# Performance work log

Measured on AMD Instinct MI355X. Metric: run time of the kernel, lower is better.

Reference implementation:

```python
import jax, jax.numpy as jnp
import numpy as np
import math


def hs_pe(x, fr, fi):
    # x: [N, c, h, w], c = cp*3; fr/fi: [max_len, cp] real/imag of freqs_cis.
    N, c, h, w = x.shape
    cp = c // 3
    xs = x.reshape(N, cp, 3, h, w)
    a, b, c3 = xs[:, :, 0], xs[:, :, 1], xs[:, :, 2]
    # rotate (a, b) as complex along h axis
    frh = fr[:h].T[None, :, :, None]  # [1, cp, h, 1]
    fih = fi[:h].T[None, :, :, None]
    a2 = a * frh - b * fih
    b2 = a * fih + b * frh
    # rotate (b2, c3) as complex along w axis
    frw = fr[:w].T[None, :, None, :]  # [1, cp, 1, w]
    fiw = fi[:w].T[None, :, None, :]
    b3 = b2 * frw - c3 * fiw
    c32 = b2 * fiw + c3 * frw
    return jnp.stack([a2, b3, c32], axis=2).reshape(N, c, h, w)


def partition(x, ws, dr):
    # OverlapDilatedWindowPartion
    B, C, H, W = x.shape
    Wsz = ws + dr
    st = Wsz // 2
    nh = math.ceil(H / Wsz)
    nw = math.ceil(W / Wsz)
    x = jnp.pad(x, ((0, 0), (0, 0), (0, nh * Wsz - H), (0, nw * Wsz - W)), mode='reflect')
    x = jnp.concatenate([x, jnp.pad(x[:, :, st:, :], ((0, 0), (0, 0), (0, st), (0, 0)), mode='reflect')], axis=0)
    x = jnp.concatenate([x, jnp.pad(x[:, :, :, st:], ((0, 0), (0, 0), (0, 0), (0, st)), mode='reflect')], axis=0)
    gb = x.shape[0]
    # 'gb c (nh h) (nw w) -> (nh nw gb) c h w'
    x = x.reshape(gb, C, nh, Wsz, nw, Wsz).transpose(2, 4, 0, 1, 3, 5).reshape(nh * nw * gb, C, Wsz, Wsz)
    return x[:, :, :ws, :ws]


def reverse(win, ws, dr, B, H, W):
    # OverlapDilatedWindowReverse
    Wsz = ws + dr
    st = Wsz // 2
    nh = math.ceil(H / Wsz)
    nw = math.ceil(W / Wsz)
    bH, bW = nh * Wsz, nw * Wsz
    win = jnp.pad(win, ((0, 0), (0, 0), (0, dr), (0, dr)))
    C = win.shape[1]
    # '(nh nw g b) c h w -> g b c (nh h) (nw w)'
    x = win.reshape(nh, nw, 4, B, C, Wsz, Wsz).transpose(2, 3, 4, 0, 5, 1, 6).reshape(4, B, C, bH, bW)
    x0 = x[0]
    x1 = jnp.pad(x[1], ((0, 0), (0, 0), (st, 0), (0, 0)))[:, :, :bH, :]
    x2 = jnp.pad(x[2], ((0, 0), (0, 0), (0, 0), (st, 0)))[:, :, :, :bW]
    x3 = jnp.pad(x[3], ((0, 0), (0, 0), (st, 0), (st, 0)))[:, :, :bH, :bW]
    return (x0 + x1 + x2 + x3)[:, :, :H, :W]


HEAD_NUM = 8
WINDOW_SIZE = 8
DILATE_RATE = 4


def setup_inputs() -> dict:
    key = jax.random.key(0)
    k1, k2, k3 = jax.random.split(key, 3)
    B, C, H, W = 1, 576, 192, 192
    x = jax.random.normal(k1, (B, C, H, W), dtype=jnp.float32)
    # rotary frequencies on the unit circle: [window_size, d//3, 2] (real, imag)
    theta = jax.random.uniform(k2, (WINDOW_SIZE, C // (3 * HEAD_NUM) // 3), dtype=jnp.float32) * (2 * np.pi)
    freqs_cis = jnp.stack([jnp.cos(theta), jnp.sin(theta)], axis=-1)
    weight = jax.random.uniform(k3, (1, 1, H, W), dtype=jnp.float32, minval=0.5, maxval=1.5)
    return {"x": x, "freqs_cis": freqs_cis, "weight": weight}


def reference(x, freqs_cis, weight):
    B, C, H, W = x.shape
    ws, dr, n = WINDOW_SIZE, DILATE_RATE, HEAD_NUM
    win = partition(x, ws, dr)  # [Nw, C, ws, ws]
    Nw = win.shape[0]
    d = C // (3 * n)
    # '(k n d)' channel split, k outer, d fastest
    qkv = win.reshape(Nw, 3, n, d, ws, ws).transpose(1, 0, 2, 3, 4, 5).reshape(3, Nw * n, d, ws, ws)
    fr, fi = freqs_cis[..., 0], freqs_cis[..., 1]
    q = hs_pe(qkv[0], fr, fi)
    k = hs_pe(qkv[1], fr, fi)
    v = qkv[2]
    def toseq(t):
        return t.reshape(Nw * n, d, ws * ws).transpose(0, 2, 1)  # [Nw*n, L, d]
    q, k, v = toseq(q), toseq(k), toseq(v)
    scale = jnp.sqrt(jnp.asarray(d, q.dtype))
    attn = jax.nn.softmax(jnp.einsum('nld,nmd->nlm', q, k) / scale, axis=-1)
    out = jnp.einsum('nlm,nmd->nld', attn, v)
    # '(Nw n) (h w) d -> Nw (n d) h w'
    out = out.reshape(Nw, n, ws, ws, d).transpose(0, 1, 4, 2, 3).reshape(Nw, n * d, ws, ws)
    out = reverse(out, ws, dr, B, H, W)
    return out / weight
```

## Files before the change

### kernel.cpp

```cpp
#include <hip/hip_runtime.h>

#define HW 36864
#define HDIM 192
#define NUNITS 8192
#define UPB 2
#define UDW 2688
#define QO 0
#define KO 768
#define VTO 1536
#define PO 0
#define O_BYTES (8192ull * 768 * 4)
#define Y_BYTES (8ull * HW * 72 * 2)

typedef __fp16 h2  __attribute__((ext_vector_type(2)));
typedef __fp16 v8h __attribute__((ext_vector_type(8)));
typedef float  v4f __attribute__((ext_vector_type(4)));

static __device__ __forceinline__ h2 pk2(float a, float b) {
    return __builtin_amdgcn_cvt_pkrtz(a, b);
}
static __device__ __forceinline__ unsigned h2u(h2 x) {
    union { h2 h; unsigned u; } c; c.h = x; return c.u;
}
static __device__ __forceinline__ h2 u2h(unsigned x) {
    union { unsigned u; h2 h; } c; c.u = x; return c.h;
}
static __device__ __forceinline__ v8h as_v8h(uint4 u) {
    union { uint4 u; v8h h; } c; c.u = u; return c.h;
}

__global__ __launch_bounds__(256)
void transpose_x(const float* __restrict__ x, uint4* __restrict__ y4) {
    const int idx  = blockIdx.x * 256 + threadIdx.x;
    const int head = idx / HW;
    const int pix  = idx - head * HW;
    const float* xp = x + (size_t)(head * 24) * HW + pix;

    unsigned o[36];
#pragma unroll
    for (int qkv = 0; qkv < 3; ++qkv)
#pragma unroll
        for (int dp = 0; dp < 12; ++dp) {
            const float a = xp[(size_t)(qkv * 192 + 2 * dp)     * HW];
            const float b = xp[(size_t)(qkv * 192 + 2 * dp + 1) * HW];
            o[qkv * 12 + dp] = h2u(pk2(a, b));
        }
    uint4* dst = y4 + (size_t)idx * 9;
#pragma unroll
    for (int j = 0; j < 9; ++j) dst[j] = *(const uint4*)&o[4 * j];
}

__global__ __launch_bounds__(128, 4)
void attn_mfma(const float* __restrict__ x,
               const uint4* __restrict__ y4,
               const float* __restrict__ fc,
               const float* __restrict__ wgt,
               float* __restrict__ out,
               unsigned* __restrict__ wsO)
{
    __shared__ unsigned lds[UPB * UDW];
    __shared__ float frs[64], fis[64];
    __shared__ unsigned zblk[4];

    const int wave = threadIdx.x >> 6;
    const int lane = threadIdx.x & 63;
    const int gid  = blockIdx.x * UPB + wave;
    const int head = gid & 7;
    const int wi   = gid >> 3;
    const int g    = wi & 3;
    const int iw   = (wi >> 2) & 15;
    const int ih   = wi >> 6;

    unsigned* uld = &lds[wave * UDW];

    if (threadIdx.x < 64) {
        float2 t = ((const float2*)fc)[threadIdx.x];
        frs[threadIdx.x] = t.x; fis[threadIdx.x] = t.y;
    } else if (threadIdx.x < 68) {
        zblk[threadIdx.x - 64] = 0;
    }
    __syncthreads();

    const int r = lane >> 3, col = lane & 7;
    const int h0 = ih * 12 + r, w0 = iw * 12 + col;
    int in_h = h0 + ((g & 1) ? 6 : 0); if (in_h >= HDIM) in_h = 2 * HDIM - 2 - in_h;
    int in_w = w0 + ((g & 2) ? 6 : 0); if (in_w >= HDIM) in_w = 2 * HDIM - 2 - in_w;

    float q[24], k[24], v[24];
    if (y4) {
        const uint4* yb = y4 + ((size_t)head * HW + (size_t)in_h * HDIM + in_w) * 9;
        uint4 qa = yb[0], qb = yb[1], qc = yb[2];
        uint4 ka = yb[3], kb = yb[4], kc = yb[5];
        uint4 va = yb[6], vb = yb[7], vc = yb[8];
#pragma unroll
        for (int j = 0; j < 4; ++j) {
            h2 t;
            t = u2h(((const unsigned*)&qa)[j]); q[2*j]    = (float)t[0]; q[2*j+1]    = (float)t[1];
            t = u2h(((const unsigned*)&qb)[j]); q[8+2*j]  = (float)t[0]; q[8+2*j+1]  = (float)t[1];
            t = u2h(((const unsigned*)&qc)[j]); q[16+2*j] = (float)t[0]; q[16+2*j+1] = (float)t[1];
            t = u2h(((const unsigned*)&ka)[j]); k[2*j]    = (float)t[0]; k[2*j+1]    = (float)t[1];
            t = u2h(((const unsigned*)&kb)[j]); k[8+2*j]  = (float)t[0]; k[8+2*j+1]  = (float)t[1];
            t = u2h(((const unsigned*)&kc)[j]); k[16+2*j] = (float)t[0]; k[16+2*j+1] = (float)t[1];
            t = u2h(((const unsigned*)&va)[j]); v[2*j]    = (float)t[0]; v[2*j+1]    = (float)t[1];
            t = u2h(((const unsigned*)&vb)[j]); v[8+2*j]  = (float)t[0]; v[8+2*j+1]  = (float)t[1];
            t = u2h(((const unsigned*)&vc)[j]); v[16+2*j] = (float)t[0]; v[16+2*j+1] = (float)t[1];
        }
    } else {
        const float* xb = x + (size_t)(head * 24) * HW + in_h * HDIM + in_w;
#pragma unroll
        for (int dd = 0; dd < 24; ++dd) q[dd] = xb[(size_t)dd * HW];
#pragma unroll
        for (int dd = 0; dd < 24; ++dd) k[dd] = xb[(size_t)dd * HW + (size_t)192 * HW];
#pragma unroll
        for (int dd = 0; dd < 24; ++dd) v[dd] = xb[(size_t)dd * HW + (size_t)384 * HW];
    }

#pragma unroll
    for (int p = 0; p < 8; ++p) {
        const float frr = frs[r * 8 + p],   fir = fis[r * 8 + p];
        const float frc = frs[col * 8 + p], fic = fis[col * 8 + p];
        {
            float a = q[3*p], b = q[3*p+1], c3 = q[3*p+2];
            float b2 = a * fir + b * frr;
            q[3*p]   = a * frr - b * fir;
            q[3*p+1] = b2 * frc - c3 * fic;
            q[3*p+2] = b2 * fic + c3 * frc;
        }
        {
            float a = k[3*p], b = k[3*p+1], c3 = k[3*p+2];
            float b2 = a * fir + b * frr;
            k[3*p]   = a * frr - b * fir;
            k[3*p+1] = b2 * frc - c3 * fic;
            k[3*p+2] = b2 * fic + c3 * frc;
        }
    }

    {
        const float sc = 0.29448903f;
        uint2* qw = (uint2*)&uld[QO + lane * 12];
        uint2* kw = (uint2*)&uld[KO + lane * 12];
#pragma unroll
        for (int j = 0; j < 3; ++j) {
            qw[2*j]   = make_uint2(h2u(pk2(q[8*j]*sc,   q[8*j+1]*sc)),
                                   h2u(pk2(q[8*j+2]*sc, q[8*j+3]*sc)));
            qw[2*j+1] = make_uint2(h2u(pk2(q[8*j+4]*sc, q[8*j+5]*sc)),
                                   h2u(pk2(q[8*j+6]*sc, q[8*j+7]*sc)));
            kw[2*j]   = make_uint2(h2u(pk2(k[8*j],   k[8*j+1])),
                                   h2u(pk2(k[8*j+2], k[8*j+3])));
            kw[2*j+1] = make_uint2(h2u(pk2(k[8*j+4], k[8*j+5])),
                                   h2u(pk2(k[8*j+6], k[8*j+7])));
        }
    }
    {
#pragma unroll
        for (int i = 0; i < 5; ++i) {
            int idx = lane + i * 64;
            if (idx < 288) uld[VTO + 24 * 36 + idx] = 0;
        }
        __fp16* vt = (__fp16*)&uld[VTO];
        vt[24 * 72 + lane] = (__fp16)1.0f;
#pragma unroll
        for (int dd = 0; dd < 24; ++dd) vt[dd * 72 + lane] = (__fp16)v[dd];
    }
    asm volatile("" ::: "memory");

    const int qq = lane >> 4, l15 = lane & 15;
    v8h Qf[4], Kf[4];
#pragma unroll
    for (int t = 0; t < 4; ++t) {
        const unsigned* qa = (qq < 3) ? &uld[QO + (16*t + l15)*12 + 4*qq] : zblk;
        const unsigned* ka = (qq < 3) ? &uld[KO + (16*t + l15)*12 + 4*qq] : zblk;
        Qf[t] = as_v8h(*(const uint4*)qa);
        Kf[t] = as_v8h(*(const uint4*)ka);
    }
    v8h Vf[2][2];
#pragma unroll
    for (int dt = 0; dt < 2; ++dt)
#pragma unroll
        for (int ks = 0; ks < 2; ++ks)
            Vf[dt][ks] = as_v8h(*(const uint4*)&uld[VTO + (16*dt + l15)*36 + 16*ks + 4*qq]);

#pragma unroll
    for (int tn = 0; tn < 4; ++tn) {
#pragma unroll
        for (int tm = 0; tm < 4; ++tm) {
            v4f c = {0.f, 0.f, 0.f, 0.f};
            c = __builtin_amdgcn_mfma_f32_16x16x32_f16(Kf[tn], Qf[tm], c, 0, 0, 0);
            uint2 w = make_uint2(h2u(pk2(exp2f(c[0]), exp2f(c[1]))),
                                 h2u(pk2(exp2f(c[2]), exp2f(c[3]))));
            *(uint2*)&uld[PO + (16*tm + l15)*36 + 8*tn + 2*qq] = w;
        }
    }

    v4f O[2][4];
#pragma unroll
    for (int dt = 0; dt < 2; ++dt)
#pragma unroll
        for (int lt = 0; lt < 4; ++lt)
            O[dt][lt] = (v4f){0.f, 0.f, 0.f, 0.f};
#pragma unroll
    for (int lt = 0; lt < 4; ++lt) {
#pragma unroll
        for (int ks = 0; ks < 2; ++ks) {
            v8h Pf = as_v8h(*(const uint4*)&uld[PO + (16*lt + l15)*36 + 16*ks + 4*qq]);
            O[0][lt] = __builtin_amdgcn_mfma_f32_16x16x32_f16(Vf[0][ks], Pf, O[0][lt], 0, 0, 0);
            O[1][lt] = __builtin_amdgcn_mfma_f32_16x16x32_f16(Vf[1][ks], Pf, O[1][lt], 0, 0, 0);
        }
    }

    float inv[4];
#pragma unroll
    for (int lt = 0; lt < 4; ++lt)
        inv[lt] = 1.0f / __shfl(O[1][lt][0], 32 + l15, 64);

    if (wsO) {
        unsigned* wb = wsO + (size_t)gid * 768;
#pragma unroll
        for (int lt = 0; lt < 4; ++lt) {
            const int   l  = 16*lt + l15;
            const float sc = inv[lt];
            wb[(2*qq+0) * 64 + l] = h2u(pk2(O[0][lt][0]*sc, O[0][lt][1]*sc));
            wb[(2*qq+1) * 64 + l] = h2u(pk2(O[0][lt][2]*sc, O[0][lt][3]*sc));
            if (qq < 2) {
                wb[(8+2*qq)   * 64 + l] = h2u(pk2(O[1][lt][0]*sc, O[1][lt][1]*sc));
                wb[(8+2*qq+1) * 64 + l] = h2u(pk2(O[1][lt][2]*sc, O[1][lt][3]*sc));
            }
        }
    } else {
#pragma unroll
        for (int lt = 0; lt < 4; ++lt) {
            const int l  = 16*lt + l15;
            const int oh = ih * 12 + (l >> 3) + ((g & 1) ? 6 : 0);
            const int ow = iw * 12 + (l & 7)  + ((g & 2) ? 6 : 0);
            if (oh < HDIM && ow < HDIM) {
                const float sc = inv[lt] / wgt[oh * HDIM + ow];
                float* ob = out + (size_t)(head * 24) * HW + oh * HDIM + ow;
#pragma unroll
                for (int rg = 0; rg < 4; ++rg)
                    atomicAdd(ob + (size_t)(4*qq + rg) * HW, O[0][lt][rg] * sc);
                if (qq < 2) {
#pragma unroll
                    for (int rg = 0; rg < 4; ++rg)
                        atomicAdd(ob + (size_t)(16 + 4*qq + rg) * HW, O[1][lt][rg] * sc);
                }
            }
        }
    }
}

__global__ __launch_bounds__(256)
void merge_out(const unsigned* __restrict__ wsO,
               const float* __restrict__ wgt,
               float* __restrict__ out)
{
    const int idx = blockIdx.x * 256 + threadIdx.x;
    const int c   = idx / HW;
    const int pix = idx - c * HW;
    const int h   = pix / HDIM;
    const int w   = pix - h * HDIM;
    const int head = c / 24;
    const int d    = c - head * 24;
    const int dp = d >> 1, hi = d & 1;

    float acc = 0.f;
#pragma unroll
    for (int g = 0; g < 4; ++g) {
        const int hh = h - ((g & 1) ? 6 : 0);
        const int ww = w - ((g & 2) ? 6 : 0);
        if (hh < 0 || ww < 0) continue;
        const int ih = hh / 12, r  = hh - ih * 12;
        const int iw = ww / 12, cw = ww - iw * 12;
        if (r >= 8 || cw >= 8) continue;
        const int unit = ((ih * 16 + iw) * 4 + g) * 8 + head;
        const unsigned u = wsO[(size_t)unit * 768 + dp * 64 + r * 8 + cw];
        acc += (float)u2h(u)[hi];
    }
    out[idx] = acc / wgt[pix];
}

extern "C" void kernel_launch(void* const* d_in, const int* in_sizes, int n_in,
                              void* d_out, int out_size, void* d_ws, size_t ws_size,
                              hipStream_t stream) {
    const float* x   = (const float*)d_in[0];
    const float* fc  = (const float*)d_in[1];
    const float* wgt = (const float*)d_in[2];
    float* out = (float*)d_out;

    const bool full  = ws_size >= O_BYTES + Y_BYTES;
    const bool ypath = full || ws_size >= Y_BYTES;
    unsigned* wsO = full ? (unsigned*)d_ws : nullptr;
    uint4*    y4  = full ? (uint4*)((char*)d_ws + O_BYTES)
                         : (ypath ? (uint4*)d_ws : nullptr);

    if (!full)
        (void)hipMemsetAsync(out, 0, (size_t)out_size * sizeof(float), stream);
    if (ypath)
        transpose_x<<<8 * HW / 256, 256, 0, stream>>>(x, y4);
    attn_mfma<<<NUNITS / UPB, UPB * 64, 0, stream>>>(x, y4, fc, wgt, out, wsO);
    if (full)
        merge_out<<<192 * HW / 256, 256, 0, stream>>>(wsO, wgt, out);
}
```

Measured before the change: 190.2 us.

## Use planar fp16 staging layout, native exp2, and pairwise merge output

Measured after the change: 172.1 us. 9.5% less time.

```diff
diff --git a/kernel.cpp b/kernel.cpp
--- a/kernel.cpp
+++ b/kernel.cpp
@@ -45,9 +45,9 @@
             const float b = xp[(size_t)(qkv * 192 + 2 * dp + 1) * HW];
             o[qkv * 12 + dp] = h2u(pk2(a, b));
         }
-    uint4* dst = y4 + (size_t)idx * 9;
-#pragma unroll
-    for (int j = 0; j < 9; ++j) dst[j] = *(const uint4*)&o[4 * j];
+    uint4* dst = y4 + (size_t)head * 9 * HW + pix;
+#pragma unroll
+    for (int j = 0; j < 9; ++j) dst[(size_t)j * HW] = *(const uint4*)&o[4 * j];
 }
 
 __global__ __launch_bounds__(128, 4)
@@ -88,10 +88,10 @@
 
     float q[24], k[24], v[24];
     if (y4) {
-        const uint4* yb = y4 + ((size_t)head * HW + (size_t)in_h * HDIM + in_w) * 9;
-        uint4 qa = yb[0], qb = yb[1], qc = yb[2];
-        uint4 ka = yb[3], kb = yb[4], kc = yb[5];
-        uint4 va = yb[6], vb = yb[7], vc = yb[8];
+        const uint4* yb = y4 + (size_t)head * 9 * HW + (size_t)in_h * HDIM + in_w;
+        uint4 qa = yb[0],        qb = yb[(size_t)HW],     qc = yb[(size_t)2 * HW];
+        uint4 ka = yb[(size_t)3 * HW], kb = yb[(size_t)4 * HW], kc = yb[(size_t)5 * HW];
+        uint4 va = yb[(size_t)6 * HW], vb = yb[(size_t)7 * HW], vc = yb[(size_t)8 * HW];
 #pragma unroll
         for (int j = 0; j < 4; ++j) {
             h2 t;
@@ -186,8 +186,10 @@
         for (int tm = 0; tm < 4; ++tm) {
             v4f c = {0.f, 0.f, 0.f, 0.f};
             c = __builtin_amdgcn_mfma_f32_16x16x32_f16(Kf[tn], Qf[tm], c, 0, 0, 0);
-            uint2 w = make_uint2(h2u(pk2(exp2f(c[0]), exp2f(c[1]))),
-                                 h2u(pk2(exp2f(c[2]), exp2f(c[3]))));
+            uint2 w = make_uint2(h2u(pk2(__builtin_amdgcn_exp2f(c[0]),
+                                         __builtin_amdgcn_exp2f(c[1]))),
+                                 h2u(pk2(__builtin_amdgcn_exp2f(c[2]),
+                                         __builtin_amdgcn_exp2f(c[3]))));
             *(uint2*)&uld[PO + (16*tm + l15)*36 + 8*tn + 2*qq] = w;
         }
     }
@@ -254,15 +256,14 @@
                float* __restrict__ out)
 {
     const int idx = blockIdx.x * 256 + threadIdx.x;
-    const int c   = idx / HW;
-    const int pix = idx - c * HW;
+    const int p   = idx / HW;
+    const int pix = idx - p * HW;
     const int h   = pix / HDIM;
     const int w   = pix - h * HDIM;
-    const int head = c / 24;
-    const int d    = c - head * 24;
-    const int dp = d >> 1, hi = d & 1;
-
-    float acc = 0.f;
+    const int head = p / 12;
+    const int dp   = p - head * 12;
+
+    float a0 = 0.f, a1 = 0.f;
 #pragma unroll
     for (int g = 0; g < 4; ++g) {
         const int hh = h - ((g & 1) ? 6 : 0);
@@ -272,10 +273,14 @@
         const int iw = ww / 12, cw = ww - iw * 12;
         if (r >= 8 || cw >= 8) continue;
         const int unit = ((ih * 16 + iw) * 4 + g) * 8 + head;
-        const unsigned u = wsO[(size_t)unit * 768 + dp * 64 + r * 8 + cw];
-        acc += (float)u2h(u)[hi];
-    }
-    out[idx] = acc / wgt[pix];
+        const h2 t = u2h(wsO[(size_t)unit * 768 + dp * 64 + r * 8 + cw]);
+        a0 += (float)t[0];
+        a1 += (float)t[1];
+    }
+    const float wv = wgt[pix];
+    const size_t c0 = (size_t)(head * 24 + 2 * dp) * HW + pix;
+    out[c0]      = a0 / wv;
+    out[c0 + HW] = a1 / wv;
 }
 
 extern "C" void kernel_launch(void* const* d_in, const int* in_sizes, int n_in,
@@ -298,5 +303,5 @@
         transpose_x<<<8 * HW / 256, 256, 0, stream>>>(x, y4);
     attn_mfma<<<NUNITS / UPB, UPB * 64, 0, stream>>>(x, y4, fc, wgt, out, wsO);
     if (full)
-        merge_out<<<192 * HW / 256, 256, 0, stream>>>(wsO, wgt, out);
-}
+        merge_out<<<96 * HW / 256, 256, 0, stream>>>(wsO, wgt, out);
+}
```
